# Kernel tuning notes

Hardware: AMD Instinct MI355X
Metric: run time of the kernel (lower is better)

## Reference

```python
import jax, jax.numpy as jnp
import numpy as np

N_NODES = 50000
N_EDGES = 800000
N_GRAPHS = 64
IN_DIM = 128
HID = 64
HEADS = 4
LAT = 32
BN_EPS = 1e-5


def setup_inputs() -> dict:
    key = jax.random.key(0)
    ks = jax.random.split(key, 16)
    x = jax.random.normal(ks[0], (N_NODES, IN_DIM), jnp.float32)
    edge_index = jax.random.randint(ks[1], (2, N_EDGES), 0, N_NODES, dtype=jnp.int64)
    batch = jnp.sort(jax.random.randint(ks[2], (N_NODES,), 0, N_GRAPHS, dtype=jnp.int64))

    def lin(k, fan_in, shape):
        return (jax.random.normal(k, shape, jnp.float32) / np.sqrt(fan_in)).astype(jnp.float32)

    d = {"x": x, "edge_index": edge_index, "batch": batch}
    dims = [IN_DIM, HID, HID]
    i = 3
    for l, din in enumerate(dims):
        d[f"Wl{l}"] = lin(ks[i], din, (din, HEADS * HID)); i += 1
        d[f"Wr{l}"] = lin(ks[i], din, (din, HEADS * HID)); i += 1
        d[f"att{l}"] = lin(ks[i], HID, (HEADS, HID)); i += 1
        d[f"b{l}"] = jnp.zeros((HID,), jnp.float32)
    d["bn_gamma"] = jnp.ones((HID,), jnp.float32)
    d["bn_beta"] = jnp.zeros((HID,), jnp.float32)
    d["fc_W"] = lin(ks[i], HID, (LAT, HID)); i += 1
    d["fc_b"] = jnp.zeros((LAT,), jnp.float32)
    return d


def _gatv2_conv(x, Wl, Wr, att, b, src, dst):
    # PyG GATv2Conv, concat=False: mean over heads. src -> dst message flow.
    n = x.shape[0]
    H, D = att.shape
    xl = (x @ Wl).reshape(n, H, D)   # source-side transform
    xr = (x @ Wr).reshape(n, H, D)   # target-side transform
    e = jax.nn.leaky_relu(xl[src] + xr[dst], 0.2)        # [E, H, D]
    logits = jnp.einsum('ehd,hd->eh', e, att)            # [E, H]
    # segment softmax over incoming edges of each dst node
    m = jax.ops.segment_max(logits, dst, num_segments=n)
    p = jnp.exp(logits - m[dst])
    denom = jax.ops.segment_sum(p, dst, num_segments=n)
    alpha = p / (denom[dst] + 1e-16)                     # [E, H]
    out = jax.ops.segment_sum(alpha[..., None] * xl[src], dst, num_segments=n)  # [N, H, D]
    return out.mean(axis=1) + b


def reference(x, edge_index, batch, Wl0, Wr0, att0, b0, Wl1, Wr1, att1, b1,
              Wl2, Wr2, att2, b2, bn_gamma, bn_beta, fc_W, fc_b):
    src, dst = edge_index[0], edge_index[1]
    h = x
    for (Wl, Wr, att, b) in ((Wl0, Wr0, att0, b0), (Wl1, Wr1, att1, b1), (Wl2, Wr2, att2, b2)):
        h = _gatv2_conv(h, Wl, Wr, att, b, src, dst)
        h = jax.nn.leaky_relu(h, 0.1)
        # dropout omitted (deterministic reference / eval semantics)
    pooled = jax.ops.segment_sum(h, batch, num_segments=N_GRAPHS)  # [G, HID]
    mean = pooled.mean(axis=0)
    var = pooled.var(axis=0)  # biased variance, matches BN training normalization
    y = (pooled - mean) / jnp.sqrt(var + BN_EPS) * bn_gamma + bn_beta
    return y @ fc_W.T + fc_b
```

## Files before the change

kernel.cpp:

```cpp
#include <hip/hip_runtime.h>
#include <hip/hip_bf16.h>
#include <math.h>

#define N_NODES 50000
#define N_EDGES 800000
#define N_GRAPHS 64
#define IN_DIM 128
#define HID 64
#define HEADS 4
#define LAT 32
#define SCAN_BLOCKS ((N_NODES + 255) / 256)

typedef __attribute__((ext_vector_type(8))) short bf16x8;
typedef __attribute__((ext_vector_type(4))) float floatx4;
typedef __attribute__((ext_vector_type(2))) float f32x2;

__device__ inline unsigned short f2bf(float f) {
    unsigned u = __float_as_uint(f);
    return (unsigned short)((u + 0x7fffu + ((u >> 16) & 1u)) >> 16);
}

__device__ inline f32x2 bfpair(unsigned u) {
    f32x2 r;
    r.x = __uint_as_float(u << 16);
    r.y = __uint_as_float(u & 0xffff0000u);
    return r;
}

__global__ __launch_bounds__(256) void deg_kernel(const int* __restrict__ dsts,
                                                  int* __restrict__ cnt, int E) {
    int e = blockIdx.x * 256 + threadIdx.x;
    if (e < E) atomicAdd(&cnt[dsts[e]], 1);
}

__global__ __launch_bounds__(256) void sum_kernel(const int* __restrict__ cnt,
                                                  int* __restrict__ bsum) {
    __shared__ int s[256];
    int i = blockIdx.x * 256 + threadIdx.x;
    s[threadIdx.x] = (i < N_NODES) ? cnt[i] : 0;
    __syncthreads();
    for (int off = 128; off; off >>= 1) {
        if (threadIdx.x < off) s[threadIdx.x] += s[threadIdx.x + off];
        __syncthreads();
    }
    if (threadIdx.x == 0) bsum[blockIdx.x] = s[0];
}

__global__ __launch_bounds__(256) void scan_blocks_kernel(const int* __restrict__ bsum,
                                                          int* __restrict__ boffs,
                                                          int* __restrict__ offs_end) {
    __shared__ int buf[256];
    int t = threadIdx.x;
    int v = (t < SCAN_BLOCKS) ? bsum[t] : 0;
    buf[t] = v;
    __syncthreads();
    #pragma unroll
    for (int off = 1; off < 256; off <<= 1) {
        int tmp = (t >= off) ? buf[t - off] : 0;
        __syncthreads();
        buf[t] += tmp;
        __syncthreads();
    }
    if (t < SCAN_BLOCKS) boffs[t] = buf[t] - v;
    if (t == 255) *offs_end = buf[255];
}

__global__ __launch_bounds__(256) void scan_final_kernel(int* __restrict__ cnt,
                                                         const int* __restrict__ boffs,
                                                         int* __restrict__ offs) {
    __shared__ int buf[256];
    int t = threadIdx.x;
    int i = blockIdx.x * 256 + t;
    int v = (i < N_NODES) ? cnt[i] : 0;
    if (i < N_NODES) cnt[i] = 0;
    buf[t] = v;
    __syncthreads();
    #pragma unroll
    for (int off = 1; off < 256; off <<= 1) {
        int tmp = (t >= off) ? buf[t - off] : 0;
        __syncthreads();
        buf[t] += tmp;
        __syncthreads();
    }
    if (i < N_NODES) offs[i] = boffs[blockIdx.x] + buf[t] - v;
}

__global__ __launch_bounds__(256) void scatter_kernel(const int* __restrict__ srcs,
                                                      const int* __restrict__ dsts,
                                                      const int* __restrict__ offs,
                                                      int* __restrict__ cnt,
                                                      int* __restrict__ es, int E) {
    int e = blockIdx.x * 256 + threadIdx.x;
    if (e < E) {
        int d = dsts[e];
        int pos = offs[d] + atomicAdd(&cnt[d], 1);
        es[pos] = srcs[e];
    }
}

__global__ __launch_bounds__(256) void conv_kernel(const float* __restrict__ x,
                                                   unsigned* __restrict__ xbf) {
    int i = blockIdx.x * 256 + threadIdx.x;
    if (i < N_NODES * IN_DIM / 2) {
        float2 v = reinterpret_cast<const float2*>(x)[i];
        xbf[i] = (unsigned)f2bf(v.x) | ((unsigned)f2bf(v.y) << 16);
    }
}

__global__ __launch_bounds__(256) void pack3_kernel(
    const float* __restrict__ Wl0, const float* __restrict__ Wr0,
    const float* __restrict__ Wl1, const float* __restrict__ Wr1,
    const float* __restrict__ Wl2, const float* __restrict__ Wr2,
    unsigned short* __restrict__ B0, unsigned short* __restrict__ B1,
    unsigned short* __restrict__ B2) {
    int idx = blockIdx.x * 256 + threadIdx.x;
    const float *Wl, *Wr;
    unsigned short* B;
    int KC, local;
    if (idx < 65536)       { Wl = Wl0; Wr = Wr0; B = B0; KC = 4; local = idx; }
    else if (idx < 98304)  { Wl = Wl1; Wr = Wr1; B = B1; KC = 2; local = idx - 65536; }
    else                   { Wl = Wl2; Wr = Wr2; B = B2; KC = 2; local = idx - 98304; }
    int j = local & 7;
    int lane = (local >> 3) & 63;
    int rem = local >> 9;
    int kc = rem % KC;
    int tile = rem / KC;
    int k = kc * 32 + (lane >> 4) * 8 + j;
    int n = (tile & 15) * 16 + (lane & 15);
    const float* W = (tile < 16) ? Wl : Wr;
    B[local] = f2bf(W[k * 256 + n]);
}

template <int K>
__global__ __launch_bounds__(256) void gemm_mfma_kernel(
    const unsigned short* __restrict__ Abf,
    const unsigned short* __restrict__ Bpk,
    unsigned short* __restrict__ xlp,
    float* __restrict__ xr) {
    constexpr int KC = K / 32;
    constexpr int CHUNKS = 16 * K / 8;
    __shared__ short As[CHUNKS * 8];
    int br = blockIdx.x * 16;
    int t = threadIdx.x;
    if (t < CHUNKS) {
        int row = t & 15;
        int kcol = (t >> 6) * 32 + ((t >> 4) & 3) * 8;
        *reinterpret_cast<uint4*>(&As[t * 8]) =
            *reinterpret_cast<const uint4*>(&Abf[(size_t)(br + row) * K + kcol]);
    }
    __syncthreads();
    int wave = t >> 6, lane = t & 63;
    int quad = lane >> 4, l16 = lane & 15;
    bf16x8 afrag[KC];
    #pragma unroll
    for (int kc = 0; kc < KC; ++kc)
        afrag[kc] = *reinterpret_cast<const bf16x8*>(&As[((kc * 4 + quad) * 16 + l16) * 8]);
    #pragma unroll
    for (int ct = 0; ct < 8; ++ct) {
        int tile = wave * 8 + ct;
        floatx4 acc = {0.f, 0.f, 0.f, 0.f};
        #pragma unroll
        for (int kc = 0; kc < KC; ++kc) {
            bf16x8 bfrag = *reinterpret_cast<const bf16x8*>(
                &Bpk[(size_t)((tile * KC + kc) * 64 + lane) * 8]);
            acc = __builtin_amdgcn_mfma_f32_16x16x32_bf16(afrag[kc], bfrag, acc, 0, 0, 0);
        }
        if (tile < 16) {
            int col = tile * 16 + l16;
            #pragma unroll
            for (int r = 0; r < 4; ++r)
                xlp[(size_t)(br + quad * 4 + r) * 256 + col] = f2bf(acc[r]);
        } else {
            int col = (tile - 16) * 16 + l16;
            #pragma unroll
            for (int r = 0; r < 4; ++r)
                xr[(size_t)(br + quad * 4 + r) * 256 + col] = acc[r];
        }
    }
}

__global__ __launch_bounds__(256) void attn_kernel(const unsigned* __restrict__ xlp,
                                                   const float4* __restrict__ xr4,
                                                   const int* __restrict__ es,
                                                   const int* __restrict__ offs,
                                                   const float4* __restrict__ att4,
                                                   const float4* __restrict__ bias4,
                                                   float* __restrict__ hout,
                                                   unsigned* __restrict__ hbf) {
    int node = blockIdx.x * 4 + (threadIdx.x >> 6);
    int lane = threadIdx.x & 63;
    int beg = offs[node], end = offs[node + 1];
    float4 xr_t = xr4[(size_t)node * 64 + lane];
    float4 at_t = att4[lane];
    f32x2 xrA = {xr_t.x, xr_t.y}, xrB = {xr_t.z, xr_t.w};
    f32x2 atA = {at_t.x, at_t.y}, atB = {at_t.z, at_t.w};
    const char* xbase = (const char*)xlp;
    int laneoff = lane << 3;

    float l = 0.f;
    f32x2 accA = {0.f, 0.f}, accB = {0.f, 0.f};

    auto edge_z = [&](uint2 v, f32x2& xa, f32x2& xb) -> float {
        xa = bfpair(v.x);
        xb = bfpair(v.y);
        f32x2 ea = xa + xrA;
        f32x2 eb = xb + xrB;
        ea = __builtin_elementwise_max(ea, ea * 0.2f);
        eb = __builtin_elementwise_max(eb, eb * 0.2f);
        f32x2 zz = ea * atA;
        zz += eb * atB;
        float z = zz.x + zz.y;
        z += __shfl_xor(z, 8);
        z += __shfl_xor(z, 4);
        z += __shfl_xor(z, 2);
        z += __shfl_xor(z, 1);
        return z;
    };
    auto gather = [&](int s) -> uint2 {
        return *reinterpret_cast<const uint2*>(
            xbase + (((size_t)(unsigned)s) << 9) + laneoff);
    };

    for (int cb = beg; cb < end; cb += 64) {
        int nch = min(64, end - cb);
        int eidx = 0;
        if (lane < nch) eidx = es[cb + lane];
        int j = 0;
        for (; j + 4 <= nch; j += 4) {
            int s0 = __shfl(eidx, j);
            int s1 = __shfl(eidx, j + 1);
            int s2 = __shfl(eidx, j + 2);
            int s3 = __shfl(eidx, j + 3);
            uint2 v0 = gather(s0);
            uint2 v1 = gather(s1);
            uint2 v2 = gather(s2);
            uint2 v3 = gather(s3);
            f32x2 xa0, xb0, xa1, xb1, xa2, xb2, xa3, xb3;
            float z0 = edge_z(v0, xa0, xb0);
            float z1 = edge_z(v1, xa1, xb1);
            float z2 = edge_z(v2, xa2, xb2);
            float z3 = edge_z(v3, xa3, xb3);
            float p0 = __expf(z0);
            float p1 = __expf(z1);
            float p2 = __expf(z2);
            float p3 = __expf(z3);
            accA += p0 * xa0 + p1 * xa1 + p2 * xa2 + p3 * xa3;
            accB += p0 * xb0 + p1 * xb1 + p2 * xb2 + p3 * xb3;
            l += (p0 + p1) + (p2 + p3);
        }
        for (; j < nch; ++j) {
            int s0 = __shfl(eidx, j);
            f32x2 xa0, xb0;
            float z0 = edge_z(gather(s0), xa0, xb0);
            float p0 = __expf(z0);
            accA += p0 * xa0;
            accB += p0 * xb0;
            l += p0;
        }
    }
    float inv = 1.f / (l + 1e-16f);
    float a0 = accA.x * inv, a1 = accA.y * inv;
    float a2 = accB.x * inv, a3 = accB.y * inv;
    a0 += __shfl_xor(a0, 16); a0 += __shfl_xor(a0, 32);
    a1 += __shfl_xor(a1, 16); a1 += __shfl_xor(a1, 32);
    a2 += __shfl_xor(a2, 16); a2 += __shfl_xor(a2, 32);
    a3 += __shfl_xor(a3, 16); a3 += __shfl_xor(a3, 32);
    if (lane < 16) {
        float4 bv = bias4[lane];
        float4 o;
        o.x = 0.25f * a0 + bv.x; o.x = (o.x > 0.f) ? o.x : 0.1f * o.x;
        o.y = 0.25f * a1 + bv.y; o.y = (o.y > 0.f) ? o.y : 0.1f * o.y;
        o.z = 0.25f * a2 + bv.z; o.z = (o.z > 0.f) ? o.z : 0.1f * o.z;
        o.w = 0.25f * a3 + bv.w; o.w = (o.w > 0.f) ? o.w : 0.1f * o.w;
        if (hout)
            *reinterpret_cast<float4*>(&hout[(size_t)node * HID + lane * 4]) = o;
        if (hbf) {
            uint2 pk;
            pk.x = (unsigned)f2bf(o.x) | ((unsigned)f2bf(o.y) << 16);
            pk.y = (unsigned)f2bf(o.z) | ((unsigned)f2bf(o.w) << 16);
            *reinterpret_cast<uint2*>(&hbf[(size_t)node * 32 + lane * 2]) = pk;
        }
    }
}

__global__ __launch_bounds__(256) void pool_kernel(const float* __restrict__ hfin,
                                                   const int* __restrict__ batch,
                                                   float* __restrict__ pooled) {
    int base = blockIdx.x * 256;
    int g = threadIdx.x >> 6, lane = threadIdx.x & 63;
    int lim = min(base + 256, N_NODES);
    int cur = -1;
    float s = 0.f;
    for (int i = base + g; i < lim; i += 4) {
        int b = batch[i];
        if (b != cur) {
            if (cur >= 0) atomicAdd(&pooled[cur * HID + lane], s);
            cur = b; s = 0.f;
        }
        s += hfin[(size_t)i * HID + lane];
    }
    if (cur >= 0) atomicAdd(&pooled[cur * HID + lane], s);
}

__global__ __launch_bounds__(256) void final_kernel(const float* __restrict__ pooled,
                                                    const float* __restrict__ gamma,
                                                    const float* __restrict__ beta,
                                                    const float* __restrict__ fcW,
                                                    const float* __restrict__ fcb,
                                                    float* __restrict__ out) {
    __shared__ float P[N_GRAPHS * HID];
    __shared__ float normS[N_GRAPHS * HID];
    __shared__ float meanS[HID], rstdS[HID];
    int t = threadIdx.x;
    for (int i = t; i < N_GRAPHS * HID; i += 256) P[i] = pooled[i];
    __syncthreads();
    if (t < HID) {
        float s = 0.f;
        for (int g = 0; g < N_GRAPHS; ++g) s += P[g * HID + t];
        float mean = s / (float)N_GRAPHS;
        float v = 0.f;
        for (int g = 0; g < N_GRAPHS; ++g) {
            float dd = P[g * HID + t] - mean;
            v += dd * dd;
        }
        v /= (float)N_GRAPHS;
        meanS[t] = mean;
        rstdS[t] = rsqrtf(v + 1e-5f);
    }
    __syncthreads();
    for (int i = t; i < N_GRAPHS * HID; i += 256) {
        int d = i & 63;
        normS[i] = (P[i] - meanS[d]) * rstdS[d] * gamma[d] + beta[d];
    }
    __syncthreads();
    for (int i = t; i < N_GRAPHS * LAT; i += 256) {
        int g = i >> 5, lat = i & 31;
        float s = fcb[lat];
        for (int d = 0; d < HID; ++d) s += normS[g * HID + d] * fcW[lat * HID + d];
        out[i] = s;
    }
}

extern "C" void kernel_launch(void* const* d_in, const int* in_sizes, int n_in,
                              void* d_out, int out_size, void* d_ws, size_t ws_size,
                              hipStream_t stream) {
    const float* x      = (const float*)d_in[0];
    const int*   ei     = (const int*)d_in[1];
    const int*   batch  = (const int*)d_in[2];
    const float* Wl[3]  = {(const float*)d_in[3], (const float*)d_in[7],  (const float*)d_in[11]};
    const float* Wr[3]  = {(const float*)d_in[4], (const float*)d_in[8],  (const float*)d_in[12]};
    const float* att[3] = {(const float*)d_in[5], (const float*)d_in[9],  (const float*)d_in[13]};
    const float* bia[3] = {(const float*)d_in[6], (const float*)d_in[10], (const float*)d_in[14]};
    const float* gamma  = (const float*)d_in[15];
    const float* beta   = (const float*)d_in[16];
    const float* fcW    = (const float*)d_in[17];
    const float* fcb    = (const float*)d_in[18];
    float* out = (float*)d_out;

    char* p = (char*)d_ws;
    auto alloc = [&](size_t bytes) {
        char* r = p;
        p += (bytes + 255) & ~(size_t)255;
        return r;
    };
    unsigned* xbf   = (unsigned*)alloc((size_t)N_NODES * IN_DIM * 2);
    unsigned short* xlp = (unsigned short*)alloc((size_t)N_NODES * 256 * 2);
    float* xr       = (float*)alloc((size_t)N_NODES * 256 * 4);
    unsigned* hbf0  = (unsigned*)alloc((size_t)N_NODES * HID * 2);
    unsigned* hbf1  = (unsigned*)alloc((size_t)N_NODES * HID * 2);
    unsigned short* Bpk0 = (unsigned short*)alloc(32 * 4 * 512 * 2);
    unsigned short* Bpk1 = (unsigned short*)alloc(32 * 2 * 512 * 2);
    unsigned short* Bpk2 = (unsigned short*)alloc(32 * 2 * 512 * 2);
    int*   es      = (int*)alloc((size_t)N_EDGES * 4);
    int*   offs    = (int*)alloc((size_t)(N_NODES + 1) * 4);
    int*   cnt     = (int*)alloc((size_t)N_NODES * 4);
    int*   bsum    = (int*)alloc((size_t)SCAN_BLOCKS * 4);
    int*   boffs   = (int*)alloc((size_t)SCAN_BLOCKS * 4);
    float* pooled  = (float*)alloc((size_t)N_GRAPHS * HID * 4);
    float* hfin    = (float*)xbf;

    const int* srcs = ei;
    const int* dsts = ei + N_EDGES;

    conv_kernel<<<(N_NODES * IN_DIM / 2 + 255) / 256, 256, 0, stream>>>(x, xbf);
    pack3_kernel<<<512, 256, 0, stream>>>(Wl[0], Wr[0], Wl[1], Wr[1], Wl[2], Wr[2],
                                          Bpk0, Bpk1, Bpk2);

    hipMemsetAsync(cnt, 0, (size_t)N_NODES * 4, stream);
    int eb = (N_EDGES + 255) / 256;
    deg_kernel<<<eb, 256, 0, stream>>>(dsts, cnt, N_EDGES);
    sum_kernel<<<SCAN_BLOCKS, 256, 0, stream>>>(cnt, bsum);
    scan_blocks_kernel<<<1, 256, 0, stream>>>(bsum, boffs, &offs[N_NODES]);
    scan_final_kernel<<<SCAN_BLOCKS, 256, 0, stream>>>(cnt, boffs, offs);
    scatter_kernel<<<eb, 256, 0, stream>>>(srcs, dsts, offs, cnt, es, N_EDGES);

    int gb = N_NODES / 16;
    gemm_mfma_kernel<IN_DIM><<<gb, 256, 0, stream>>>((const unsigned short*)xbf, Bpk0, xlp, xr);
    attn_kernel<<<N_NODES / 4, 256, 0, stream>>>((const unsigned*)xlp, (const float4*)xr,
                                                 es, offs, (const float4*)att[0],
                                                 (const float4*)bia[0], nullptr, hbf0);
    gemm_mfma_kernel<HID><<<gb, 256, 0, stream>>>((const unsigned short*)hbf0, Bpk1, xlp, xr);
    attn_kernel<<<N_NODES / 4, 256, 0, stream>>>((const unsigned*)xlp, (const float4*)xr,
                                                 es, offs, (const float4*)att[1],
                                                 (const float4*)bia[1], nullptr, hbf1);
    gemm_mfma_kernel<HID><<<gb, 256, 0, stream>>>((const unsigned short*)hbf1, Bpk2, xlp, xr);
    attn_kernel<<<N_NODES / 4, 256, 0, stream>>>((const unsigned*)xlp, (const float4*)xr,
                                                 es, offs, (const float4*)att[2],
                                                 (const float4*)bia[2], hfin, nullptr);

    hipMemsetAsync(pooled, 0, (size_t)N_GRAPHS * HID * 4, stream);
    pool_kernel<<<SCAN_BLOCKS, 256, 0, stream>>>(hfin, batch, pooled);
    final_kernel<<<1, 256, 0, stream>>>(pooled, gamma, beta, fcW, fcb, out);
}
```

Before: 495.6 us.

## Process four edges per wave in attention and store xr as bf16

The attention kernel now splits each wave into four 16-lane groups, each handling a different incoming edge. Each lane covers 16 features with 32-byte gathers, and the group partial sums are reduced through shared memory at the end. The target-side transform xr is written and read as bf16 instead of fp32, which halves its memory traffic. The aim is more memory-level parallelism per wave and less per-edge shuffle overhead. In exchange it adds register pressure, shared-memory reduction work and wasted lanes when a node's degree is not a multiple of four, and bf16 xr lowers precision.

```diff
diff --git a/kernel.cpp b/kernel.cpp
--- a/kernel.cpp
+++ b/kernel.cpp
@@ -136,7 +136,7 @@
     const unsigned short* __restrict__ Abf,
     const unsigned short* __restrict__ Bpk,
     unsigned short* __restrict__ xlp,
-    float* __restrict__ xr) {
+    unsigned short* __restrict__ xrp) {
     constexpr int KC = K / 32;
     constexpr int CHUNKS = 16 * K / 8;
     __shared__ short As[CHUNKS * 8];
@@ -174,111 +174,104 @@
             int col = (tile - 16) * 16 + l16;
             #pragma unroll
             for (int r = 0; r < 4; ++r)
-                xr[(size_t)(br + quad * 4 + r) * 256 + col] = acc[r];
+                xrp[(size_t)(br + quad * 4 + r) * 256 + col] = f2bf(acc[r]);
         }
     }
 }
 
 __global__ __launch_bounds__(256) void attn_kernel(const unsigned* __restrict__ xlp,
-                                                   const float4* __restrict__ xr4,
+                                                   const unsigned* __restrict__ xrp,
                                                    const int* __restrict__ es,
                                                    const int* __restrict__ offs,
-                                                   const float4* __restrict__ att4,
-                                                   const float4* __restrict__ bias4,
+                                                   const float* __restrict__ att,
+                                                   const float* __restrict__ bias,
                                                    float* __restrict__ hout,
                                                    unsigned* __restrict__ hbf) {
-    int node = blockIdx.x * 4 + (threadIdx.x >> 6);
+    __shared__ float red[4][1024];
+    int wave = threadIdx.x >> 6;
     int lane = threadIdx.x & 63;
+    int node = blockIdx.x * 4 + wave;
+    int g = lane >> 4;
+    int s = lane & 15;
     int beg = offs[node], end = offs[node + 1];
-    float4 xr_t = xr4[(size_t)node * 64 + lane];
-    float4 at_t = att4[lane];
-    f32x2 xrA = {xr_t.x, xr_t.y}, xrB = {xr_t.z, xr_t.w};
-    f32x2 atA = {at_t.x, at_t.y}, atB = {at_t.z, at_t.w};
-    const char* xbase = (const char*)xlp;
-    int laneoff = lane << 3;
-
+
+    f32x2 xrv[8], atv[8];
+    {
+        const uint4* r4 = reinterpret_cast<const uint4*>(xrp + (size_t)node * 128);
+        uint4 a = r4[s * 2], b = r4[s * 2 + 1];
+        xrv[0] = bfpair(a.x); xrv[1] = bfpair(a.y);
+        xrv[2] = bfpair(a.z); xrv[3] = bfpair(a.w);
+        xrv[4] = bfpair(b.x); xrv[5] = bfpair(b.y);
+        xrv[6] = bfpair(b.z); xrv[7] = bfpair(b.w);
+        const float4* a4 = reinterpret_cast<const float4*>(att);
+        #pragma unroll
+        for (int k = 0; k < 4; ++k) {
+            float4 c = a4[s * 4 + k];
+            atv[2 * k]     = f32x2{c.x, c.y};
+            atv[2 * k + 1] = f32x2{c.z, c.w};
+        }
+    }
+
+    f32x2 acc[8];
+    #pragma unroll
+    for (int k = 0; k < 8; ++k) acc[k] = f32x2{0.f, 0.f};
     float l = 0.f;
-    f32x2 accA = {0.f, 0.f}, accB = {0.f, 0.f};
-
-    auto edge_z = [&](uint2 v, f32x2& xa, f32x2& xb) -> float {
-        xa = bfpair(v.x);
-        xb = bfpair(v.y);
-        f32x2 ea = xa + xrA;
-        f32x2 eb = xb + xrB;
-        ea = __builtin_elementwise_max(ea, ea * 0.2f);
-        eb = __builtin_elementwise_max(eb, eb * 0.2f);
-        f32x2 zz = ea * atA;
-        zz += eb * atB;
+    const char* xb = (const char*)xlp;
+
+    for (int cb = beg; cb < end; cb += 4) {
+        int e = cb + g;
+        int src = es[(e < end) ? e : (end - 1)];
+        const uint4* row = reinterpret_cast<const uint4*>(
+            xb + ((size_t)(unsigned)src << 9));
+        uint4 va = row[s * 2];
+        uint4 vb = row[s * 2 + 1];
+        f32x2 xv[8];
+        xv[0] = bfpair(va.x); xv[1] = bfpair(va.y);
+        xv[2] = bfpair(va.z); xv[3] = bfpair(va.w);
+        xv[4] = bfpair(vb.x); xv[5] = bfpair(vb.y);
+        xv[6] = bfpair(vb.z); xv[7] = bfpair(vb.w);
+        f32x2 zz = f32x2{0.f, 0.f};
+        #pragma unroll
+        for (int k = 0; k < 8; ++k) {
+            f32x2 t = xv[k] + xrv[k];
+            t = __builtin_elementwise_max(t, t * 0.2f);
+            zz += t * atv[k];
+        }
         float z = zz.x + zz.y;
-        z += __shfl_xor(z, 8);
-        z += __shfl_xor(z, 4);
+        z += __shfl_xor(z, 1);
         z += __shfl_xor(z, 2);
-        z += __shfl_xor(z, 1);
-        return z;
-    };
-    auto gather = [&](int s) -> uint2 {
-        return *reinterpret_cast<const uint2*>(
-            xbase + (((size_t)(unsigned)s) << 9) + laneoff);
-    };
-
-    for (int cb = beg; cb < end; cb += 64) {
-        int nch = min(64, end - cb);
-        int eidx = 0;
-        if (lane < nch) eidx = es[cb + lane];
-        int j = 0;
-        for (; j + 4 <= nch; j += 4) {
-            int s0 = __shfl(eidx, j);
-            int s1 = __shfl(eidx, j + 1);
-            int s2 = __shfl(eidx, j + 2);
-            int s3 = __shfl(eidx, j + 3);
-            uint2 v0 = gather(s0);
-            uint2 v1 = gather(s1);
-            uint2 v2 = gather(s2);
-            uint2 v3 = gather(s3);
-            f32x2 xa0, xb0, xa1, xb1, xa2, xb2, xa3, xb3;
-            float z0 = edge_z(v0, xa0, xb0);
-            float z1 = edge_z(v1, xa1, xb1);
-            float z2 = edge_z(v2, xa2, xb2);
-            float z3 = edge_z(v3, xa3, xb3);
-            float p0 = __expf(z0);
-            float p1 = __expf(z1);
-            float p2 = __expf(z2);
-            float p3 = __expf(z3);
-            accA += p0 * xa0 + p1 * xa1 + p2 * xa2 + p3 * xa3;
-            accB += p0 * xb0 + p1 * xb1 + p2 * xb2 + p3 * xb3;
-            l += (p0 + p1) + (p2 + p3);
-        }
-        for (; j < nch; ++j) {
-            int s0 = __shfl(eidx, j);
-            f32x2 xa0, xb0;
-            float z0 = edge_z(gather(s0), xa0, xb0);
-            float p0 = __expf(z0);
-            accA += p0 * xa0;
-            accB += p0 * xb0;
-            l += p0;
-        }
-    }
+        float p = (e < end) ? __expf(z) : 0.f;
+        l += p;
+        #pragma unroll
+        for (int k = 0; k < 8; ++k) acc[k] += p * xv[k];
+    }
+
+    l += __shfl_xor(l, 16);
+    l += __shfl_xor(l, 32);
     float inv = 1.f / (l + 1e-16f);
-    float a0 = accA.x * inv, a1 = accA.y * inv;
-    float a2 = accB.x * inv, a3 = accB.y * inv;
-    a0 += __shfl_xor(a0, 16); a0 += __shfl_xor(a0, 32);
-    a1 += __shfl_xor(a1, 16); a1 += __shfl_xor(a1, 32);
-    a2 += __shfl_xor(a2, 16); a2 += __shfl_xor(a2, 32);
-    a3 += __shfl_xor(a3, 16); a3 += __shfl_xor(a3, 32);
-    if (lane < 16) {
-        float4 bv = bias4[lane];
-        float4 o;
-        o.x = 0.25f * a0 + bv.x; o.x = (o.x > 0.f) ? o.x : 0.1f * o.x;
-        o.y = 0.25f * a1 + bv.y; o.y = (o.y > 0.f) ? o.y : 0.1f * o.y;
-        o.z = 0.25f * a2 + bv.z; o.z = (o.z > 0.f) ? o.z : 0.1f * o.z;
-        o.w = 0.25f * a3 + bv.w; o.w = (o.w > 0.f) ? o.w : 0.1f * o.w;
-        if (hout)
-            *reinterpret_cast<float4*>(&hout[(size_t)node * HID + lane * 4]) = o;
-        if (hbf) {
-            uint2 pk;
-            pk.x = (unsigned)f2bf(o.x) | ((unsigned)f2bf(o.y) << 16);
-            pk.y = (unsigned)f2bf(o.z) | ((unsigned)f2bf(o.w) << 16);
-            *reinterpret_cast<uint2*>(&hbf[(size_t)node * 32 + lane * 2]) = pk;
+    #pragma unroll
+    for (int k = 0; k < 8; ++k) acc[k] *= inv;
+
+    float* sl = red[wave];
+    float4* dst = reinterpret_cast<float4*>(&sl[g * 256 + s * 16]);
+    dst[0] = make_float4(acc[0].x, acc[0].y, acc[1].x, acc[1].y);
+    dst[1] = make_float4(acc[2].x, acc[2].y, acc[3].x, acc[3].y);
+    dst[2] = make_float4(acc[4].x, acc[4].y, acc[5].x, acc[5].y);
+    dst[3] = make_float4(acc[6].x, acc[6].y, acc[7].x, acc[7].y);
+    float sum = 0.f;
+    #pragma unroll
+    for (int g2 = 0; g2 < 4; ++g2)
+        #pragma unroll
+        for (int h = 0; h < 4; ++h)
+            sum += sl[g2 * 256 + h * 64 + lane];
+    float o = 0.25f * sum + bias[lane];
+    o = (o > 0.f) ? o : 0.1f * o;
+    if (hout) hout[(size_t)node * HID + lane] = o;
+    if (hbf) {
+        float o2 = __shfl_xor(o, 1);
+        if (!(lane & 1)) {
+            unsigned pk = (unsigned)f2bf(o) | ((unsigned)f2bf(o2) << 16);
+            hbf[(size_t)node * 32 + (lane >> 1)] = pk;
         }
     }
 }
@@ -365,7 +358,7 @@
     };
     unsigned* xbf   = (unsigned*)alloc((size_t)N_NODES * IN_DIM * 2);
     unsigned short* xlp = (unsigned short*)alloc((size_t)N_NODES * 256 * 2);
-    float* xr       = (float*)alloc((size_t)N_NODES * 256 * 4);
+    unsigned short* xrp = (unsigned short*)alloc((size_t)N_NODES * 256 * 2);
     unsigned* hbf0  = (unsigned*)alloc((size_t)N_NODES * HID * 2);
     unsigned* hbf1  = (unsigned*)alloc((size_t)N_NODES * HID * 2);
     unsigned short* Bpk0 = (unsigned short*)alloc(32 * 4 * 512 * 2);
@@ -395,18 +388,15 @@
     scatter_kernel<<<eb, 256, 0, stream>>>(srcs, dsts, offs, cnt, es, N_EDGES);
 
     int gb = N_NODES / 16;
-    gemm_mfma_kernel<IN_DIM><<<gb, 256, 0, stream>>>((const unsigned short*)xbf, Bpk0, xlp, xr);
-    attn_kernel<<<N_NODES / 4, 256, 0, stream>>>((const unsigned*)xlp, (const float4*)xr,
-                                                 es, offs, (const float4*)att[0],
-                                                 (const float4*)bia[0], nullptr, hbf0);
-    gemm_mfma_kernel<HID><<<gb, 256, 0, stream>>>((const unsigned short*)hbf0, Bpk1, xlp, xr);
-    attn_kernel<<<N_NODES / 4, 256, 0, stream>>>((const unsigned*)xlp, (const float4*)xr,
-                                                 es, offs, (const float4*)att[1],
-                                                 (const float4*)bia[1], nullptr, hbf1);
-    gemm_mfma_kernel<HID><<<gb, 256, 0, stream>>>((const unsigned short*)hbf1, Bpk2, xlp, xr);
-    attn_kernel<<<N_NODES / 4, 256, 0, stream>>>((const unsigned*)xlp, (const float4*)xr,
-                                                 es, offs, (const float4*)att[2],
-                                                 (const float4*)bia[2], hfin, nullptr);
+    gemm_mfma_kernel<IN_DIM><<<gb, 256, 0, stream>>>((const unsigned short*)xbf, Bpk0, xlp, xrp);
+    attn_kernel<<<N_NODES / 4, 256, 0, stream>>>((const unsigned*)xlp, (const unsigned*)xrp,
+                                                 es, offs, att[0], bia[0], nullptr, hbf0);
+    gemm_mfma_kernel<HID><<<gb, 256, 0, stream>>>((const unsigned short*)hbf0, Bpk1, xlp, xrp);
+    attn_kernel<<<N_NODES / 4, 256, 0, stream>>>((const unsigned*)xlp, (const unsigned*)xrp,
+                                                 es, offs, att[1], bia[1], nullptr, hbf1);
+    gemm_mfma_kernel<HID><<<gb, 256, 0, stream>>>((const unsigned short*)hbf1, Bpk2, xlp, xrp);
+    attn_kernel<<<N_NODES / 4, 256, 0, stream>>>((const unsigned*)xlp, (const unsigned*)xrp,
+                                                 es, offs, att[2], bia[2], hfin, nullptr);
 
     hipMemsetAsync(pooled, 0, (size_t)N_GRAPHS * HID * 4, stream);
     pool_kernel<<<SCAN_BLOCKS, 256, 0, stream>>>(hfin, batch, pooled);
```

New measurement: 540.5 us. 1.09x slower.

## Pad CSR rows to multiples of four, store xr as bf16, use DPP reductions

Applied to the files above, without the earlier changes.

The CSR edge list is rebuilt with each node's segment padded to a multiple of four, so the attention loop reads four source indices at once with an int4 load instead of going through a shuffle-based chunk loop. Padding slots are zeroed with a memset and masked out by degree. The target-side projection xr is stored as bf16 instead of fp32, halving its write and read traffic. The 16-lane dot-product reduction uses DPP row_shr moves instead of shfl_xor. The trade-offs are wasted gathers on padded slots, an extra memset of the padded buffer, and lower precision in xr.

```diff
diff --git a/kernel.cpp b/kernel.cpp
--- a/kernel.cpp
+++ b/kernel.cpp
@@ -10,6 +10,7 @@
 #define HEADS 4
 #define LAT 32
 #define SCAN_BLOCKS ((N_NODES + 255) / 256)
+#define ES_CAP 960000
 
 typedef __attribute__((ext_vector_type(8))) short bf16x8;
 typedef __attribute__((ext_vector_type(4))) float floatx4;
@@ -27,6 +28,14 @@
     return r;
 }
 
+__device__ inline float rowsum16(float x) {
+    x += __int_as_float(__builtin_amdgcn_mov_dpp(__float_as_int(x), 0x128, 0xf, 0xf, false));
+    x += __int_as_float(__builtin_amdgcn_mov_dpp(__float_as_int(x), 0x124, 0xf, 0xf, false));
+    x += __int_as_float(__builtin_amdgcn_mov_dpp(__float_as_int(x), 0x122, 0xf, 0xf, false));
+    x += __int_as_float(__builtin_amdgcn_mov_dpp(__float_as_int(x), 0x121, 0xf, 0xf, false));
+    return x;
+}
+
 __global__ __launch_bounds__(256) void deg_kernel(const int* __restrict__ dsts,
                                                   int* __restrict__ cnt, int E) {
     int e = blockIdx.x * 256 + threadIdx.x;
@@ -37,7 +46,8 @@
                                                   int* __restrict__ bsum) {
     __shared__ int s[256];
     int i = blockIdx.x * 256 + threadIdx.x;
-    s[threadIdx.x] = (i < N_NODES) ? cnt[i] : 0;
+    int c = (i < N_NODES) ? cnt[i] : 0;
+    s[threadIdx.x] = (c + 3) & ~3;
     __syncthreads();
     for (int off = 128; off; off >>= 1) {
         if (threadIdx.x < off) s[threadIdx.x] += s[threadIdx.x + off];
@@ -47,8 +57,7 @@
 }
 
 __global__ __launch_bounds__(256) void scan_blocks_kernel(const int* __restrict__ bsum,
-                                                          int* __restrict__ boffs,
-                                                          int* __restrict__ offs_end) {
+                                                          int* __restrict__ boffs) {
     __shared__ int buf[256];
     int t = threadIdx.x;
     int v = (t < SCAN_BLOCKS) ? bsum[t] : 0;
@@ -62,17 +71,17 @@
         __syncthreads();
     }
     if (t < SCAN_BLOCKS) boffs[t] = buf[t] - v;
-    if (t == 255) *offs_end = buf[255];
-}
-
-__global__ __launch_bounds__(256) void scan_final_kernel(int* __restrict__ cnt,
+}
+
+__global__ __launch_bounds__(256) void scan_final_kernel(const int* __restrict__ cnt,
                                                          const int* __restrict__ boffs,
-                                                         int* __restrict__ offs) {
+                                                         int* __restrict__ offs,
+                                                         int* __restrict__ sc) {
     __shared__ int buf[256];
     int t = threadIdx.x;
     int i = blockIdx.x * 256 + t;
-    int v = (i < N_NODES) ? cnt[i] : 0;
-    if (i < N_NODES) cnt[i] = 0;
+    int v = 0;
+    if (i < N_NODES) v = (cnt[i] + 3) & ~3;
     buf[t] = v;
     __syncthreads();
     #pragma unroll
@@ -82,18 +91,21 @@
         buf[t] += tmp;
         __syncthreads();
     }
-    if (i < N_NODES) offs[i] = boffs[blockIdx.x] + buf[t] - v;
+    if (i < N_NODES) {
+        offs[i] = boffs[blockIdx.x] + buf[t] - v;
+        sc[i] = 0;
+    }
 }
 
 __global__ __launch_bounds__(256) void scatter_kernel(const int* __restrict__ srcs,
                                                       const int* __restrict__ dsts,
                                                       const int* __restrict__ offs,
-                                                      int* __restrict__ cnt,
+                                                      int* __restrict__ sc,
                                                       int* __restrict__ es, int E) {
     int e = blockIdx.x * 256 + threadIdx.x;
     if (e < E) {
         int d = dsts[e];
-        int pos = offs[d] + atomicAdd(&cnt[d], 1);
+        int pos = offs[d] + atomicAdd(&sc[d], 1);
         es[pos] = srcs[e];
     }
 }
@@ -136,7 +148,7 @@
     const unsigned short* __restrict__ Abf,
     const unsigned short* __restrict__ Bpk,
     unsigned short* __restrict__ xlp,
-    float* __restrict__ xr) {
+    unsigned short* __restrict__ xrp) {
     constexpr int KC = K / 32;
     constexpr int CHUNKS = 16 * K / 8;
     __shared__ short As[CHUNKS * 8];
@@ -174,25 +186,27 @@
             int col = (tile - 16) * 16 + l16;
             #pragma unroll
             for (int r = 0; r < 4; ++r)
-                xr[(size_t)(br + quad * 4 + r) * 256 + col] = acc[r];
+                xrp[(size_t)(br + quad * 4 + r) * 256 + col] = f2bf(acc[r]);
         }
     }
 }
 
 __global__ __launch_bounds__(256) void attn_kernel(const unsigned* __restrict__ xlp,
-                                                   const float4* __restrict__ xr4,
+                                                   const unsigned* __restrict__ xrp,
                                                    const int* __restrict__ es,
                                                    const int* __restrict__ offs,
+                                                   const int* __restrict__ deg,
                                                    const float4* __restrict__ att4,
                                                    const float4* __restrict__ bias4,
                                                    float* __restrict__ hout,
                                                    unsigned* __restrict__ hbf) {
     int node = blockIdx.x * 4 + (threadIdx.x >> 6);
     int lane = threadIdx.x & 63;
-    int beg = offs[node], end = offs[node + 1];
-    float4 xr_t = xr4[(size_t)node * 64 + lane];
+    int beg = offs[node];
+    int end = beg + deg[node];
+    uint2 xr2 = reinterpret_cast<const uint2*>(xrp)[(size_t)node * 64 + lane];
+    f32x2 xrA = bfpair(xr2.x), xrB = bfpair(xr2.y);
     float4 at_t = att4[lane];
-    f32x2 xrA = {xr_t.x, xr_t.y}, xrB = {xr_t.z, xr_t.w};
     f32x2 atA = {at_t.x, at_t.y}, atB = {at_t.z, at_t.w};
     const char* xbase = (const char*)xlp;
     int laneoff = lane << 3;
@@ -209,55 +223,33 @@
         eb = __builtin_elementwise_max(eb, eb * 0.2f);
         f32x2 zz = ea * atA;
         zz += eb * atB;
-        float z = zz.x + zz.y;
-        z += __shfl_xor(z, 8);
-        z += __shfl_xor(z, 4);
-        z += __shfl_xor(z, 2);
-        z += __shfl_xor(z, 1);
-        return z;
+        return zz.x + zz.y;
     };
     auto gather = [&](int s) -> uint2 {
         return *reinterpret_cast<const uint2*>(
             xbase + (((size_t)(unsigned)s) << 9) + laneoff);
     };
 
-    for (int cb = beg; cb < end; cb += 64) {
-        int nch = min(64, end - cb);
-        int eidx = 0;
-        if (lane < nch) eidx = es[cb + lane];
-        int j = 0;
-        for (; j + 4 <= nch; j += 4) {
-            int s0 = __shfl(eidx, j);
-            int s1 = __shfl(eidx, j + 1);
-            int s2 = __shfl(eidx, j + 2);
-            int s3 = __shfl(eidx, j + 3);
-            uint2 v0 = gather(s0);
-            uint2 v1 = gather(s1);
-            uint2 v2 = gather(s2);
-            uint2 v3 = gather(s3);
-            f32x2 xa0, xb0, xa1, xb1, xa2, xb2, xa3, xb3;
-            float z0 = edge_z(v0, xa0, xb0);
-            float z1 = edge_z(v1, xa1, xb1);
-            float z2 = edge_z(v2, xa2, xb2);
-            float z3 = edge_z(v3, xa3, xb3);
-            float p0 = __expf(z0);
-            float p1 = __expf(z1);
-            float p2 = __expf(z2);
-            float p3 = __expf(z3);
-            accA += p0 * xa0 + p1 * xa1 + p2 * xa2 + p3 * xa3;
-            accB += p0 * xb0 + p1 * xb1 + p2 * xb2 + p3 * xb3;
-            l += (p0 + p1) + (p2 + p3);
-        }
-        for (; j < nch; ++j) {
-            int s0 = __shfl(eidx, j);
-            f32x2 xa0, xb0;
-            float z0 = edge_z(gather(s0), xa0, xb0);
-            float p0 = __expf(z0);
-            accA += p0 * xa0;
-            accB += p0 * xb0;
-            l += p0;
-        }
-    }
+    for (int cb = beg; cb < end; cb += 4) {
+        int4 s4 = *reinterpret_cast<const int4*>(&es[cb]);
+        uint2 v0 = gather(s4.x);
+        uint2 v1 = gather(s4.y);
+        uint2 v2 = gather(s4.z);
+        uint2 v3 = gather(s4.w);
+        f32x2 xa0, xb0, xa1, xb1, xa2, xb2, xa3, xb3;
+        float z0 = rowsum16(edge_z(v0, xa0, xb0));
+        float z1 = rowsum16(edge_z(v1, xa1, xb1));
+        float z2 = rowsum16(edge_z(v2, xa2, xb2));
+        float z3 = rowsum16(edge_z(v3, xa3, xb3));
+        float p0 = __expf(z0);
+        float p1 = (cb + 1 < end) ? __expf(z1) : 0.f;
+        float p2 = (cb + 2 < end) ? __expf(z2) : 0.f;
+        float p3 = (cb + 3 < end) ? __expf(z3) : 0.f;
+        accA += p0 * xa0 + p1 * xa1 + p2 * xa2 + p3 * xa3;
+        accB += p0 * xb0 + p1 * xb1 + p2 * xb2 + p3 * xb3;
+        l += (p0 + p1) + (p2 + p3);
+    }
+
     float inv = 1.f / (l + 1e-16f);
     float a0 = accA.x * inv, a1 = accA.y * inv;
     float a2 = accB.x * inv, a3 = accB.y * inv;
@@ -365,15 +357,16 @@
     };
     unsigned* xbf   = (unsigned*)alloc((size_t)N_NODES * IN_DIM * 2);
     unsigned short* xlp = (unsigned short*)alloc((size_t)N_NODES * 256 * 2);
-    float* xr       = (float*)alloc((size_t)N_NODES * 256 * 4);
+    unsigned short* xrp = (unsigned short*)alloc((size_t)N_NODES * 256 * 2);
     unsigned* hbf0  = (unsigned*)alloc((size_t)N_NODES * HID * 2);
     unsigned* hbf1  = (unsigned*)alloc((size_t)N_NODES * HID * 2);
     unsigned short* Bpk0 = (unsigned short*)alloc(32 * 4 * 512 * 2);
     unsigned short* Bpk1 = (unsigned short*)alloc(32 * 2 * 512 * 2);
     unsigned short* Bpk2 = (unsigned short*)alloc(32 * 2 * 512 * 2);
-    int*   es      = (int*)alloc((size_t)N_EDGES * 4);
-    int*   offs    = (int*)alloc((size_t)(N_NODES + 1) * 4);
+    int*   es      = (int*)alloc((size_t)ES_CAP * 4);
+    int*   offs    = (int*)alloc((size_t)N_NODES * 4);
     int*   cnt     = (int*)alloc((size_t)N_NODES * 4);
+    int*   sc      = (int*)alloc((size_t)N_NODES * 4);
     int*   bsum    = (int*)alloc((size_t)SCAN_BLOCKS * 4);
     int*   boffs   = (int*)alloc((size_t)SCAN_BLOCKS * 4);
     float* pooled  = (float*)alloc((size_t)N_GRAPHS * HID * 4);
@@ -387,25 +380,26 @@
                                           Bpk0, Bpk1, Bpk2);
 
     hipMemsetAsync(cnt, 0, (size_t)N_NODES * 4, stream);
+    hipMemsetAsync(es, 0, (size_t)ES_CAP * 4, stream);
     int eb = (N_EDGES + 255) / 256;
     deg_kernel<<<eb, 256, 0, stream>>>(dsts, cnt, N_EDGES);
     sum_kernel<<<SCAN_BLOCKS, 256, 0, stream>>>(cnt, bsum);
-    scan_blocks_kernel<<<1, 256, 0, stream>>>(bsum, boffs, &offs[N_NODES]);
-    scan_final_kernel<<<SCAN_BLOCKS, 256, 0, stream>>>(cnt, boffs, offs);
-    scatter_kernel<<<eb, 256, 0, stream>>>(srcs, dsts, offs, cnt, es, N_EDGES);
+    scan_blocks_kernel<<<1, 256, 0, stream>>>(bsum, boffs);
+    scan_final_kernel<<<SCAN_BLOCKS, 256, 0, stream>>>(cnt, boffs, offs, sc);
+    scatter_kernel<<<eb, 256, 0, stream>>>(srcs, dsts, offs, sc, es, N_EDGES);
 
     int gb = N_NODES / 16;
-    gemm_mfma_kernel<IN_DIM><<<gb, 256, 0, stream>>>((const unsigned short*)xbf, Bpk0, xlp, xr);
-    attn_kernel<<<N_NODES / 4, 256, 0, stream>>>((const unsigned*)xlp, (const float4*)xr,
-                                                 es, offs, (const float4*)att[0],
+    gemm_mfma_kernel<IN_DIM><<<gb, 256, 0, stream>>>((const unsigned short*)xbf, Bpk0, xlp, xrp);
+    attn_kernel<<<N_NODES / 4, 256, 0, stream>>>((const unsigned*)xlp, (const unsigned*)xrp,
+                                                 es, offs, cnt, (const float4*)att[0],
                                                  (const float4*)bia[0], nullptr, hbf0);
-    gemm_mfma_kernel<HID><<<gb, 256, 0, stream>>>((const unsigned short*)hbf0, Bpk1, xlp, xr);
-    attn_kernel<<<N_NODES / 4, 256, 0, stream>>>((const unsigned*)xlp, (const float4*)xr,
-                                                 es, offs, (const float4*)att[1],
+    gemm_mfma_kernel<HID><<<gb, 256, 0, stream>>>((const unsigned short*)hbf0, Bpk1, xlp, xrp);
+    attn_kernel<<<N_NODES / 4, 256, 0, stream>>>((const unsigned*)xlp, (const unsigned*)xrp,
+                                                 es, offs, cnt, (const float4*)att[1],
                                                  (const float4*)bia[1], nullptr, hbf1);
-    gemm_mfma_kernel<HID><<<gb, 256, 0, stream>>>((const unsigned short*)hbf1, Bpk2, xlp, xr);
-    attn_kernel<<<N_NODES / 4, 256, 0, stream>>>((const unsigned*)xlp, (const float4*)xr,
-                                                 es, offs, (const float4*)att[2],
+    gemm_mfma_kernel<HID><<<gb, 256, 0, stream>>>((const unsigned short*)hbf1, Bpk2, xlp, xrp);
+    attn_kernel<<<N_NODES / 4, 256, 0, stream>>>((const unsigned*)xlp, (const unsigned*)xrp,
+                                                 es, offs, cnt, (const float4*)att[2],
                                                  (const float4*)bia[2], hfin, nullptr);
 
     hipMemsetAsync(pooled, 0, (size_t)N_GRAPHS * HID * 4, stream);
```

Measured after the change: 487.9 us. No clear change (-1.6%).
